# Optimization experiments

Hardware: AMD Instinct MI355X
Metric: run time of the kernel (lower is better)

## Reference

```python
import jax, jax.numpy as jnp
import numpy as np

P = 2.0  # exponent from init kwarg p


def _segment_mean(vals, idx, n):
    # scatter-mean with zero for empty segments (matches torch_scatter reduce='mean')
    s = jax.ops.segment_sum(vals, idx, num_segments=n)
    c = jax.ops.segment_sum(jnp.ones((vals.shape[0], 1), vals.dtype), idx, num_segments=n)
    return s / jnp.maximum(c, 1.0)


def setup_inputs() -> dict:
    key = jax.random.key(0)
    ks = jax.random.split(key, 6)
    N, E, nhid, heads = 100000, 3200000, 64, 4
    X = jax.random.normal(ks[0], (N, nhid), dtype=jnp.float32)
    edge_index = jax.random.randint(ks[1], (2, E), 0, N, dtype=jnp.int32)
    s1 = 1.0 / np.sqrt(nhid)
    W_self = jax.random.normal(ks[2], (nhid, nhid), dtype=jnp.float32) * s1
    W_neigh = jax.random.normal(ks[3], (nhid, nhid), dtype=jnp.float32) * s1
    b_conv = jnp.zeros((nhid,), dtype=jnp.float32)
    s2 = 1.0 / np.sqrt(2 * nhid)
    Qw = jax.random.normal(ks[4], (heads, 2 * nhid, nhid // heads), dtype=jnp.float32) * s2
    Qb = jnp.zeros((heads, nhid // heads), dtype=jnp.float32)
    return {"X": X, "edge_index": edge_index, "W_self": W_self,
            "W_neigh": W_neigh, "b_conv": b_conv, "Qw": Qw, "Qb": Qb}


def reference(X, edge_index, W_self, W_neigh, b_conv, Qw, Qb):
    N = X.shape[0]
    src, dst = edge_index[0], edge_index[1]
    # GraphSAGE conv: self-linear + linear over mean of neighbor features, then ReLU
    agg = _segment_mean(X[src], dst, N)                     # [N, nhid]
    X2 = jax.nn.relu(X @ W_self + agg @ W_neigh + b_conv)   # [N, nhid]
    # gather both edge endpoints and concat
    ef = jnp.concatenate([X2[src], X2[dst]], axis=1)        # [E, 2*nhid]
    # per-head small linear, abs^p, heads concatenated -> [E, nhid]
    h = jnp.einsum('ef,hfd->ehd', ef, Qw) + Qb              # [E, heads, nhid/heads]
    h = (jnp.abs(h) ** P).reshape(ef.shape[0], -1)
    # scatter-mean by source node, tanh
    gg = jnp.tanh(_segment_mean(h, src, N))                 # [N, nhid]
    return gg
```

## Files before the change

### kernel.cpp

```cpp
#include <hip/hip_runtime.h>
#include <math.h>

#define NHID 64
#define NPB 512
#define NPB_SHIFT 9
#define MAXB 256
#define CAP 20480
#define CHUNK 8192

__device__ __forceinline__ float bf_lo(unsigned u) { return __uint_as_float(u << 16); }
__device__ __forceinline__ float bf_hi(unsigned u) { return __uint_as_float(u & 0xffff0000u); }
__device__ __forceinline__ unsigned f2bf(float f) {
    unsigned u = __float_as_uint(f);
    return (u + 0x7fffu + ((u >> 16) & 1u)) >> 16;
}

__global__ __launch_bounds__(256) void k_bucketA(const int* __restrict__ src,
                                                 const int* __restrict__ dst,
                                                 unsigned int* __restrict__ buf0,
                                                 unsigned int* __restrict__ buf1,
                                                 int* __restrict__ btail0,
                                                 int* __restrict__ btail1,
                                                 int E, int nB, int nChunks) {
    int side  = blockIdx.x & 1;
    int chunk = blockIdx.x >> 1;
    const int* key = side ? src : dst;
    const int* pay = side ? dst : src;
    unsigned int* buf = side ? buf1 : buf0;
    int* btail = side ? btail1 : btail0;

    __shared__ int h[MAXB], b[MAXB];
    int tid = threadIdx.x;
    for (int i = tid; i < nB; i += 256) h[i] = 0;
    __syncthreads();
    int e0 = chunk * CHUNK;
    for (int i = tid; i < CHUNK / 4; i += 256) {
        int e = e0 + i * 4;
        if (e + 3 < E) {
            int4 k4 = ((const int4*)(key + e0))[i];
            atomicAdd(&h[k4.x >> NPB_SHIFT], 1);
            atomicAdd(&h[k4.y >> NPB_SHIFT], 1);
            atomicAdd(&h[k4.z >> NPB_SHIFT], 1);
            atomicAdd(&h[k4.w >> NPB_SHIFT], 1);
        } else {
            for (int j = 0; j < 4; ++j) {
                int e2 = e + j;
                if (e2 < E) atomicAdd(&h[key[e2] >> NPB_SHIFT], 1);
            }
        }
    }
    __syncthreads();
    for (int i = tid; i < nB; i += 256) {
        int c = h[i];
        b[i] = c ? atomicAdd(&btail[i], c) : 0;
        h[i] = 0;
    }
    __syncthreads();
    for (int i = tid; i < CHUNK / 4; i += 256) {
        int e = e0 + i * 4;
        if (e + 3 < E) {
            int4 k4 = ((const int4*)(key + e0))[i];
            int4 p4 = ((const int4*)(pay + e0))[i];
            int bb, r;
            bb = k4.x >> NPB_SHIFT; r = atomicAdd(&h[bb], 1) + b[bb];
            if (r < CAP) buf[(size_t)bb * CAP + r] = ((unsigned)p4.x << NPB_SHIFT) | (unsigned)(k4.x & (NPB - 1));
            bb = k4.y >> NPB_SHIFT; r = atomicAdd(&h[bb], 1) + b[bb];
            if (r < CAP) buf[(size_t)bb * CAP + r] = ((unsigned)p4.y << NPB_SHIFT) | (unsigned)(k4.y & (NPB - 1));
            bb = k4.z >> NPB_SHIFT; r = atomicAdd(&h[bb], 1) + b[bb];
            if (r < CAP) buf[(size_t)bb * CAP + r] = ((unsigned)p4.z << NPB_SHIFT) | (unsigned)(k4.z & (NPB - 1));
            bb = k4.w >> NPB_SHIFT; r = atomicAdd(&h[bb], 1) + b[bb];
            if (r < CAP) buf[(size_t)bb * CAP + r] = ((unsigned)p4.w << NPB_SHIFT) | (unsigned)(k4.w & (NPB - 1));
        } else {
            for (int j = 0; j < 4; ++j) {
                int e2 = e + j;
                if (e2 < E) {
                    int k = key[e2], p = pay[e2];
                    int bb = k >> NPB_SHIFT;
                    int r = atomicAdd(&h[bb], 1) + b[bb];
                    if (r < CAP) buf[(size_t)bb * CAP + r] = ((unsigned)p << NPB_SHIFT) | (unsigned)(k & (NPB - 1));
                }
            }
        }
    }
}

__global__ __launch_bounds__(256) void k_bscan(const int* __restrict__ btail0,
                                               const int* __restrict__ btail1,
                                               int* __restrict__ boff0, int* __restrict__ boff1,
                                               int* __restrict__ off0, int* __restrict__ off1,
                                               int nB, int N) {
    __shared__ int sd[256];
    int tid = threadIdx.x;
    int v = (tid < nB) ? min(btail0[tid], CAP) : 0;
    sd[tid] = v; __syncthreads();
    for (int o = 1; o < 256; o <<= 1) {
        int t = (tid >= o) ? sd[tid - o] : 0; __syncthreads();
        sd[tid] += t; __syncthreads();
    }
    if (tid < nB) boff0[tid] = sd[tid] - v;
    if (tid == 255) off0[N] = sd[255];
    __syncthreads();
    v = (tid < nB) ? min(btail1[tid], CAP) : 0;
    sd[tid] = v; __syncthreads();
    for (int o = 1; o < 256; o <<= 1) {
        int t = (tid >= o) ? sd[tid - o] : 0; __syncthreads();
        sd[tid] += t; __syncthreads();
    }
    if (tid < nB) boff1[tid] = sd[tid] - v;
    if (tid == 255) off1[N] = sd[255];
}

__global__ __launch_bounds__(512) void k_bucket_csr(const unsigned int* __restrict__ buf0,
                                                    const unsigned int* __restrict__ buf1,
                                                    const int* __restrict__ btail0,
                                                    const int* __restrict__ btail1,
                                                    const int* __restrict__ boff0,
                                                    const int* __restrict__ boff1,
                                                    int* __restrict__ off0, int* __restrict__ off1,
                                                    int* __restrict__ csr0, int* __restrict__ csr1,
                                                    int N) {
    int side = blockIdx.x & 1;
    int b = blockIdx.x >> 1;
    const unsigned int* buf = (side ? buf1 : buf0) + (size_t)b * CAP;
    int cnt_b = min((side ? btail1 : btail0)[b], CAP);
    int boff  = (side ? boff1 : boff0)[b];
    int* off  = side ? off1 : off0;
    int* csr  = side ? csr1 : csr0;
    __shared__ int cnt[NPB];
    __shared__ int scn[NPB];
    __shared__ int cur[NPB];
    int tid = threadIdx.x;
    cnt[tid] = 0;
    __syncthreads();
    for (int i = tid; i < cnt_b; i += 512)
        atomicAdd(&cnt[buf[i] & (NPB - 1)], 1);
    __syncthreads();
    int v = cnt[tid];
    scn[tid] = v; __syncthreads();
    for (int o = 1; o < 512; o <<= 1) {
        int t = (tid >= o) ? scn[tid - o] : 0; __syncthreads();
        scn[tid] += t; __syncthreads();
    }
    int base = boff + scn[tid] - v;
    cur[tid] = base;
    int node = (b << NPB_SHIFT) + tid;
    if (node < N) off[node] = base;
    __syncthreads();
    for (int i = tid; i < cnt_b; i += 512) {
        unsigned int u = buf[i];
        int pos = atomicAdd(&cur[u & (NPB - 1)], 1);
        csr[pos] = (int)(u >> NPB_SHIFT);
    }
}

__global__ __launch_bounds__(256) void k_xcast(const float* __restrict__ X,
                                               unsigned* __restrict__ Xb, int total8) {
    int i = blockIdx.x * 256 + threadIdx.x;
    if (i >= total8) return;
    const float4* Xv = (const float4*)X;
    float4 f0 = Xv[(size_t)i * 2];
    float4 f1 = Xv[(size_t)i * 2 + 1];
    uint4 p;
    p.x = f2bf(f0.x) | (f2bf(f0.y) << 16);
    p.y = f2bf(f0.z) | (f2bf(f0.w) << 16);
    p.z = f2bf(f1.x) | (f2bf(f1.y) << 16);
    p.w = f2bf(f1.z) | (f2bf(f1.w) << 16);
    ((uint4*)Xb)[i] = p;
}

__global__ __launch_bounds__(256) void k_agg(const unsigned* __restrict__ Xb,
                                             const int* __restrict__ off_dst,
                                             const int* __restrict__ csr_dst,
                                             float* __restrict__ agg, int N) {
    int lane = threadIdx.x & 63;
    int node = blockIdx.x * 4 + (threadIdx.x >> 6);
    if (node >= N) return;
    int grp = lane >> 3, col8 = lane & 7;
    const uint4* Xb4 = (const uint4*)Xb;
    int s0 = off_dst[node], s1 = off_dst[node + 1];
    float4 accA = make_float4(0.f, 0.f, 0.f, 0.f);
    float4 accB = make_float4(0.f, 0.f, 0.f, 0.f);
    for (int base = s0; base < s1; base += 64) {
        int cnt = min(64, s1 - base);
        int idx = (base + lane < s1) ? csr_dst[base + lane] : 0;
        int jfull = cnt & ~15;
        for (int j = 0; j < jfull; j += 16) {
            int m0 = __shfl(idx, j + grp);
            int m1 = __shfl(idx, j + 8 + grp);
            uint4 u0 = Xb4[(size_t)m0 * 8 + col8];
            uint4 u1 = Xb4[(size_t)m1 * 8 + col8];
            accA.x += bf_lo(u0.x); accA.y += bf_hi(u0.x);
            accA.z += bf_lo(u0.y); accA.w += bf_hi(u0.y);
            accB.x += bf_lo(u0.z); accB.y += bf_hi(u0.z);
            accB.z += bf_lo(u0.w); accB.w += bf_hi(u0.w);
            accA.x += bf_lo(u1.x); accA.y += bf_hi(u1.x);
            accA.z += bf_lo(u1.y); accA.w += bf_hi(u1.y);
            accB.x += bf_lo(u1.z); accB.y += bf_hi(u1.z);
            accB.z += bf_lo(u1.w); accB.w += bf_hi(u1.w);
        }
        if (jfull < cnt) {
            int q0 = jfull + grp, q1 = jfull + 8 + grp;
            int m0 = __shfl(idx, q0);
            int m1 = __shfl(idx, q1);
            float f0 = (q0 < cnt) ? 1.f : 0.f; if (q0 >= cnt) m0 = 0;
            float f1 = (q1 < cnt) ? 1.f : 0.f; if (q1 >= cnt) m1 = 0;
            uint4 u0 = Xb4[(size_t)m0 * 8 + col8];
            uint4 u1 = Xb4[(size_t)m1 * 8 + col8];
            accA.x += f0 * bf_lo(u0.x); accA.y += f0 * bf_hi(u0.x);
            accA.z += f0 * bf_lo(u0.y); accA.w += f0 * bf_hi(u0.y);
            accB.x += f0 * bf_lo(u0.z); accB.y += f0 * bf_hi(u0.z);
            accB.z += f0 * bf_lo(u0.w); accB.w += f0 * bf_hi(u0.w);
            accA.x += f1 * bf_lo(u1.x); accA.y += f1 * bf_hi(u1.x);
            accA.z += f1 * bf_lo(u1.y); accA.w += f1 * bf_hi(u1.y);
            accB.x += f1 * bf_lo(u1.z); accB.y += f1 * bf_hi(u1.z);
            accB.z += f1 * bf_lo(u1.w); accB.w += f1 * bf_hi(u1.w);
        }
    }
    #pragma unroll
    for (int d = 8; d < 64; d <<= 1) {
        accA.x += __shfl_xor(accA.x, d); accA.y += __shfl_xor(accA.y, d);
        accA.z += __shfl_xor(accA.z, d); accA.w += __shfl_xor(accA.w, d);
        accB.x += __shfl_xor(accB.x, d); accB.y += __shfl_xor(accB.y, d);
        accB.z += __shfl_xor(accB.z, d); accB.w += __shfl_xor(accB.w, d);
    }
    if (grp == 0) {
        int deg = s1 - s0;
        float inv = 1.f / (float)max(deg, 1);
        float4 r0 = make_float4(accA.x * inv, accA.y * inv, accA.z * inv, accA.w * inv);
        float4 r1 = make_float4(accB.x * inv, accB.y * inv, accB.z * inv, accB.w * inv);
        ((float4*)agg)[(size_t)node * 16 + col8 * 2]     = r0;
        ((float4*)agg)[(size_t)node * 16 + col8 * 2 + 1] = r1;
    }
}

__global__ __launch_bounds__(256) void k_phaseA(const float* __restrict__ X,
                                                const float* agg,
                                                const float* __restrict__ Ws,
                                                const float* __restrict__ Wn,
                                                const float* __restrict__ bconv,
                                                float* X2, int N) {
    __shared__ float sWs[4096];
    __shared__ float sWn[4096];
    __shared__ float sb[64];
    int tid = threadIdx.x;
    for (int i = tid; i < 4096; i += 256) {
        sWs[i] = Ws[i];
        sWn[i] = Wn[i];
    }
    if (tid < 64) sb[tid] = bconv[tid];
    __syncthreads();

    int n = blockIdx.x * 64 + (tid >> 2);
    if (n >= N) return;
    int wb = (tid & 3) << 2;
    const float4* ws4 = (const float4*)sWs;
    const float4* wn4 = (const float4*)sWn;
    const float4* bv  = (const float4*)sb;
    const float4* Xv  = (const float4*)(X + (size_t)n * NHID);
    const float4* Gv  = (const float4*)(agg + (size_t)n * NHID);
    float4 a0 = bv[wb], a1 = bv[wb + 1], a2 = bv[wb + 2], a3 = bv[wb + 3];
    #pragma unroll 2
    for (int q = 0; q < 16; ++q) {
        float4 xq = Xv[q];
        float4 gq = Gv[q];
        float xs[4] = {xq.x, xq.y, xq.z, xq.w};
        float gs[4] = {gq.x, gq.y, gq.z, gq.w};
        #pragma unroll
        for (int j = 0; j < 4; ++j) {
            int k16 = (4 * q + j) * 16 + wb;
            float4 w0 = ws4[k16], w1 = ws4[k16 + 1], w2 = ws4[k16 + 2], w3 = ws4[k16 + 3];
            float4 m0 = wn4[k16], m1 = wn4[k16 + 1], m2 = wn4[k16 + 2], m3 = wn4[k16 + 3];
            float xj = xs[j], gj = gs[j];
            a0.x += xj * w0.x + gj * m0.x; a0.y += xj * w0.y + gj * m0.y;
            a0.z += xj * w0.z + gj * m0.z; a0.w += xj * w0.w + gj * m0.w;
            a1.x += xj * w1.x + gj * m1.x; a1.y += xj * w1.y + gj * m1.y;
            a1.z += xj * w1.z + gj * m1.z; a1.w += xj * w1.w + gj * m1.w;
            a2.x += xj * w2.x + gj * m2.x; a2.y += xj * w2.y + gj * m2.y;
            a2.z += xj * w2.z + gj * m2.z; a2.w += xj * w2.w + gj * m2.w;
            a3.x += xj * w3.x + gj * m3.x; a3.y += xj * w3.y + gj * m3.y;
            a3.z += xj * w3.z + gj * m3.z; a3.w += xj * w3.w + gj * m3.w;
        }
    }
    float4* out = (float4*)(X2 + (size_t)n * NHID);
    out[wb]     = make_float4(fmaxf(a0.x, 0.f), fmaxf(a0.y, 0.f), fmaxf(a0.z, 0.f), fmaxf(a0.w, 0.f));
    out[wb + 1] = make_float4(fmaxf(a1.x, 0.f), fmaxf(a1.y, 0.f), fmaxf(a1.z, 0.f), fmaxf(a1.w, 0.f));
    out[wb + 2] = make_float4(fmaxf(a2.x, 0.f), fmaxf(a2.y, 0.f), fmaxf(a2.z, 0.f), fmaxf(a2.w, 0.f));
    out[wb + 3] = make_float4(fmaxf(a3.x, 0.f), fmaxf(a3.y, 0.f), fmaxf(a3.z, 0.f), fmaxf(a3.w, 0.f));
}

__global__ __launch_bounds__(256) void k_repackB(const float* __restrict__ Qw,
                                                 float* __restrict__ W2) {
    int i = blockIdx.x * 256 + threadIdx.x;
    if (i >= 8192) return;
    int f = i >> 7, c = i & 127;
    float v;
    if (c < 64) v = Qw[(c >> 4) * 2048 + f * 16 + (c & 15)];
    else { int cc = c - 64; v = Qw[(cc >> 4) * 2048 + (64 + f) * 16 + (cc & 15)]; }
    W2[i] = v;
}

__global__ __launch_bounds__(256) void k_phaseB(const float* __restrict__ X2,
                                                const float* __restrict__ W2,
                                                const float* __restrict__ Qb,
                                                float* __restrict__ aOut,
                                                unsigned* __restrict__ bOut, int N) {
    __shared__ float sW[8192];
    int tid = threadIdx.x;
    for (int i = tid; i < 8192; i += 256) sW[i] = W2[i];
    __syncthreads();

    int n = blockIdx.x * 32 + (tid >> 3);
    if (n >= N) return;
    int part = tid & 7;
    int wb = part << 2;
    const float4* w4 = (const float4*)sW;
    float4 a0, a1, a2, a3;
    if (part < 4) {
        const float4* qv = (const float4*)Qb;
        a0 = qv[wb]; a1 = qv[wb + 1]; a2 = qv[wb + 2]; a3 = qv[wb + 3];
    } else {
        a0 = a1 = a2 = a3 = make_float4(0.f, 0.f, 0.f, 0.f);
    }
    const float4* Xv = (const float4*)(X2 + (size_t)n * NHID);
    #pragma unroll 2
    for (int q = 0; q < 16; ++q) {
        float4 xq = Xv[q];
        float xs[4] = {xq.x, xq.y, xq.z, xq.w};
        #pragma unroll
        for (int j = 0; j < 4; ++j) {
            int f32b = (4 * q + j) * 32 + wb;
            float4 w0 = w4[f32b], w1 = w4[f32b + 1], w2 = w4[f32b + 2], w3 = w4[f32b + 3];
            float xj = xs[j];
            a0.x += xj * w0.x; a0.y += xj * w0.y; a0.z += xj * w0.z; a0.w += xj * w0.w;
            a1.x += xj * w1.x; a1.y += xj * w1.y; a1.z += xj * w1.z; a1.w += xj * w1.w;
            a2.x += xj * w2.x; a2.y += xj * w2.y; a2.z += xj * w2.z; a2.w += xj * w2.w;
            a3.x += xj * w3.x; a3.y += xj * w3.y; a3.z += xj * w3.z; a3.w += xj * w3.w;
        }
    }
    if (part < 4) {
        float4* outp = (float4*)(aOut + (size_t)n * NHID) + wb;
        outp[0] = a0; outp[1] = a1; outp[2] = a2; outp[3] = a3;
    } else {
        uint4 p0, p1;
        p0.x = f2bf(a0.x) | (f2bf(a0.y) << 16);
        p0.y = f2bf(a0.z) | (f2bf(a0.w) << 16);
        p0.z = f2bf(a1.x) | (f2bf(a1.y) << 16);
        p0.w = f2bf(a1.z) | (f2bf(a1.w) << 16);
        p1.x = f2bf(a2.x) | (f2bf(a2.y) << 16);
        p1.y = f2bf(a2.z) | (f2bf(a2.w) << 16);
        p1.z = f2bf(a3.x) | (f2bf(a3.y) << 16);
        p1.w = f2bf(a3.z) | (f2bf(a3.w) << 16);
        uint4* outp = (uint4*)bOut + (size_t)n * 8 + (part - 4) * 2;
        outp[0] = p0; outp[1] = p1;
    }
}

__global__ __launch_bounds__(256) void k_final(const float* __restrict__ aF,
                                               const unsigned* __restrict__ bFb,
                                               const int* __restrict__ off_src,
                                               const int* __restrict__ csr_src,
                                               float* __restrict__ out, int N) {
    int lane = threadIdx.x & 63;
    int node = blockIdx.x * 4 + (threadIdx.x >> 6);
    if (node >= N) return;
    int grp = lane >> 3, col8 = lane & 7;
    const uint4* Bv = (const uint4*)bFb;
    const float4* Av = (const float4*)aF;
    float4 avA = Av[(size_t)node * 16 + col8 * 2];
    float4 avB = Av[(size_t)node * 16 + col8 * 2 + 1];
    int s0 = off_src[node], s1 = off_src[node + 1];
    float4 accA = make_float4(0.f, 0.f, 0.f, 0.f);
    float4 accB = make_float4(0.f, 0.f, 0.f, 0.f);
    for (int base = s0; base < s1; base += 64) {
        int cnt = min(64, s1 - base);
        int idx = (base + lane < s1) ? csr_src[base + lane] : 0;
        int jfull = cnt & ~15;
        for (int j = 0; j < jfull; j += 16) {
            int m0 = __shfl(idx, j + grp);
            int m1 = __shfl(idx, j + 8 + grp);
            uint4 u0 = Bv[(size_t)m0 * 8 + col8];
            uint4 u1 = Bv[(size_t)m1 * 8 + col8];
            float t;
            t = avA.x + bf_lo(u0.x); accA.x += t * t;
            t = avA.y + bf_hi(u0.x); accA.y += t * t;
            t = avA.z + bf_lo(u0.y); accA.z += t * t;
            t = avA.w + bf_hi(u0.y); accA.w += t * t;
            t = avB.x + bf_lo(u0.z); accB.x += t * t;
            t = avB.y + bf_hi(u0.z); accB.y += t * t;
            t = avB.z + bf_lo(u0.w); accB.z += t * t;
            t = avB.w + bf_hi(u0.w); accB.w += t * t;
            t = avA.x + bf_lo(u1.x); accA.x += t * t;
            t = avA.y + bf_hi(u1.x); accA.y += t * t;
            t = avA.z + bf_lo(u1.y); accA.z += t * t;
            t = avA.w + bf_hi(u1.y); accA.w += t * t;
            t = avB.x + bf_lo(u1.z); accB.x += t * t;
            t = avB.y + bf_hi(u1.z); accB.y += t * t;
            t = avB.z + bf_lo(u1.w); accB.z += t * t;
            t = avB.w + bf_hi(u1.w); accB.w += t * t;
        }
        if (jfull < cnt) {
            int q0 = jfull + grp, q1 = jfull + 8 + grp;
            int m0 = __shfl(idx, q0);
            int m1 = __shfl(idx, q1);
            float f0 = (q0 < cnt) ? 1.f : 0.f; if (q0 >= cnt) m0 = 0;
            float f1 = (q1 < cnt) ? 1.f : 0.f; if (q1 >= cnt) m1 = 0;
            uint4 u0 = Bv[(size_t)m0 * 8 + col8];
            uint4 u1 = Bv[(size_t)m1 * 8 + col8];
            float t;
            t = avA.x + bf_lo(u0.x); accA.x += f0 * t * t;
            t = avA.y + bf_hi(u0.x); accA.y += f0 * t * t;
            t = avA.z + bf_lo(u0.y); accA.z += f0 * t * t;
            t = avA.w + bf_hi(u0.y); accA.w += f0 * t * t;
            t = avB.x + bf_lo(u0.z); accB.x += f0 * t * t;
            t = avB.y + bf_hi(u0.z); accB.y += f0 * t * t;
            t = avB.z + bf_lo(u0.w); accB.z += f0 * t * t;
            t = avB.w + bf_hi(u0.w); accB.w += f0 * t * t;
            t = avA.x + bf_lo(u1.x); accA.x += f1 * t * t;
            t = avA.y + bf_hi(u1.x); accA.y += f1 * t * t;
            t = avA.z + bf_lo(u1.y); accA.z += f1 * t * t;
            t = avA.w + bf_hi(u1.y); accA.w += f1 * t * t;
            t = avB.x + bf_lo(u1.z); accB.x += f1 * t * t;
            t = avB.y + bf_hi(u1.z); accB.y += f1 * t * t;
            t = avB.z + bf_lo(u1.w); accB.z += f1 * t * t;
            t = avB.w + bf_hi(u1.w); accB.w += f1 * t * t;
        }
    }
    #pragma unroll
    for (int d = 8; d < 64; d <<= 1) {
        accA.x += __shfl_xor(accA.x, d); accA.y += __shfl_xor(accA.y, d);
        accA.z += __shfl_xor(accA.z, d); accA.w += __shfl_xor(accA.w, d);
        accB.x += __shfl_xor(accB.x, d); accB.y += __shfl_xor(accB.y, d);
        accB.z += __shfl_xor(accB.z, d); accB.w += __shfl_xor(accB.w, d);
    }
    if (grp == 0) {
        int deg = s1 - s0;
        float inv = 1.f / (float)max(deg, 1);
        float4 r0 = make_float4(tanhf(accA.x * inv), tanhf(accA.y * inv),
                                tanhf(accA.z * inv), tanhf(accA.w * inv));
        float4 r1 = make_float4(tanhf(accB.x * inv), tanhf(accB.y * inv),
                                tanhf(accB.z * inv), tanhf(accB.w * inv));
        ((float4*)out)[(size_t)node * 16 + col8 * 2]     = r0;
        ((float4*)out)[(size_t)node * 16 + col8 * 2 + 1] = r1;
    }
}

extern "C" void kernel_launch(void* const* d_in, const int* in_sizes, int n_in,
                              void* d_out, int out_size, void* d_ws, size_t ws_size,
                              hipStream_t stream) {
    const float* X      = (const float*)d_in[0];
    const int*   ei     = (const int*)d_in[1];
    const float* Wself  = (const float*)d_in[2];
    const float* Wneigh = (const float*)d_in[3];
    const float* bconv  = (const float*)d_in[4];
    const float* Qw     = (const float*)d_in[5];
    const float* Qb     = (const float*)d_in[6];

    int N = in_sizes[0] / NHID;
    int E = in_sizes[1] / 2;
    const int* src = ei;
    const int* dst = ei + E;
    int nB = (N + NPB - 1) >> NPB_SHIFT;
    int nChunks = (E + CHUNK - 1) / CHUNK;

    char* ws = (char*)d_ws;
    size_t bufBytes = (size_t)MAXB * CAP * 4;
    size_t NH4 = (size_t)N * NHID * 4;
    size_t NH2 = (size_t)N * NHID * 2;
    unsigned int* buf0 = (unsigned int*)(ws);
    unsigned int* buf1 = (unsigned int*)(ws + bufBytes);
    float*    aggF = (float*)(ws);
    float*    aF   = (float*)(ws + NH4);
    unsigned* bFb  = (unsigned*)(ws + 2 * NH4);
    unsigned* Xb   = (unsigned*)(ws + 2 * NH4 + NH2);
    size_t pos = 3 * NH4;
    if (pos < 2 * bufBytes) pos = 2 * bufBytes;
    pos = (pos + 255) & ~(size_t)255;
    auto alloc = [&](size_t bytes) -> void* {
        void* p = ws + pos;
        pos = (pos + bytes + 255) & ~(size_t)255;
        return p;
    };
    int* csr0   = (int*)alloc((size_t)E * 4);
    int* csr1   = (int*)alloc((size_t)E * 4);
    int* off0   = (int*)alloc((size_t)(N + 1) * 4);
    int* off1   = (int*)alloc((size_t)(N + 1) * 4);
    int* btail0 = (int*)alloc((size_t)MAXB * 4);
    int* btail1 = (int*)alloc((size_t)MAXB * 4);
    int* boff0  = (int*)alloc((size_t)MAXB * 4);
    int* boff1  = (int*)alloc((size_t)MAXB * 4);
    float* W2   = (float*)alloc((size_t)8192 * 4);
    (void)ws_size; (void)n_in; (void)out_size;

    hipMemsetAsync(btail0, 0, (size_t)2 * MAXB * 4, stream);

    k_bucketA<<<nChunks * 2, 256, 0, stream>>>(src, dst, buf0, buf1, btail0, btail1,
                                               E, nB, nChunks);
    k_bscan<<<1, 256, 0, stream>>>(btail0, btail1, boff0, boff1, off0, off1, nB, N);
    k_repackB<<<32, 256, 0, stream>>>(Qw, W2);
    k_xcast<<<(N * 8 + 255) / 256, 256, 0, stream>>>(X, Xb, N * 8);
    k_bucket_csr<<<nB * 2, 512, 0, stream>>>(buf0, buf1, btail0, btail1,
                                             boff0, boff1, off0, off1, csr0, csr1, N);
    k_agg<<<(N + 3) / 4, 256, 0, stream>>>(Xb, off0, csr0, aggF, N);
    k_phaseA<<<(N + 63) / 64, 256, 0, stream>>>(X, aggF, Wself, Wneigh, bconv, aggF, N);
    k_phaseB<<<(N + 31) / 32, 256, 0, stream>>>(aggF, W2, Qb, aF, bFb, N);
    k_final<<<(N + 3) / 4, 256, 0, stream>>>(aF, bFb, off1, csr1, (float*)d_out, N);
}
```

Baseline: 329.6 us.

## Store X2 and per-node head projections in bf16 and unroll gathers by four

The ReLU output X2 and the per-node 'a' projection are now stored as packed bf16 instead of fp32, which halves intermediate traffic between phaseA, phaseB and the final edge kernel. The neighbor gather loops in k_agg and k_final now process 32 edges per iteration instead of 16, which puts more loads in flight per wave. The unused nChunks argument is dropped, and X2 is written to its own buffer instead of overwriting the aggregate in place. The cost is extra bf16 rounding on X2 and on the 'a' term before squaring, which adds numerical error.

```diff
diff --git a/kernel.cpp b/kernel.cpp
--- a/kernel.cpp
+++ b/kernel.cpp
@@ -21,7 +21,7 @@
                                                  unsigned int* __restrict__ buf1,
                                                  int* __restrict__ btail0,
                                                  int* __restrict__ btail1,
-                                                 int E, int nB, int nChunks) {
+                                                 int E, int nB) {
     int side  = blockIdx.x & 1;
     int chunk = blockIdx.x >> 1;
     const int* key = side ? src : dst;
@@ -168,6 +168,17 @@
     ((uint4*)Xb)[i] = p;
 }
 
+#define AGG_ACC(u) \
+    accA.x += bf_lo(u.x); accA.y += bf_hi(u.x); \
+    accA.z += bf_lo(u.y); accA.w += bf_hi(u.y); \
+    accB.x += bf_lo(u.z); accB.y += bf_hi(u.z); \
+    accB.z += bf_lo(u.w); accB.w += bf_hi(u.w);
+#define AGG_ACCM(u, f) \
+    accA.x += f * bf_lo(u.x); accA.y += f * bf_hi(u.x); \
+    accA.z += f * bf_lo(u.y); accA.w += f * bf_hi(u.y); \
+    accB.x += f * bf_lo(u.z); accB.y += f * bf_hi(u.z); \
+    accB.z += f * bf_lo(u.w); accB.w += f * bf_hi(u.w);
+
 __global__ __launch_bounds__(256) void k_agg(const unsigned* __restrict__ Xb,
                                              const int* __restrict__ off_dst,
                                              const int* __restrict__ csr_dst,
@@ -183,37 +194,33 @@
     for (int base = s0; base < s1; base += 64) {
         int cnt = min(64, s1 - base);
         int idx = (base + lane < s1) ? csr_dst[base + lane] : 0;
-        int jfull = cnt & ~15;
-        for (int j = 0; j < jfull; j += 16) {
+        int j = 0;
+        for (; j + 32 <= cnt; j += 32) {
             int m0 = __shfl(idx, j + grp);
             int m1 = __shfl(idx, j + 8 + grp);
+            int m2 = __shfl(idx, j + 16 + grp);
+            int m3 = __shfl(idx, j + 24 + grp);
             uint4 u0 = Xb4[(size_t)m0 * 8 + col8];
             uint4 u1 = Xb4[(size_t)m1 * 8 + col8];
-            accA.x += bf_lo(u0.x); accA.y += bf_hi(u0.x);
-            accA.z += bf_lo(u0.y); accA.w += bf_hi(u0.y);
-            accB.x += bf_lo(u0.z); accB.y += bf_hi(u0.z);
-            accB.z += bf_lo(u0.w); accB.w += bf_hi(u0.w);
-            accA.x += bf_lo(u1.x); accA.y += bf_hi(u1.x);
-            accA.z += bf_lo(u1.y); accA.w += bf_hi(u1.y);
-            accB.x += bf_lo(u1.z); accB.y += bf_hi(u1.z);
-            accB.z += bf_lo(u1.w); accB.w += bf_hi(u1.w);
-        }
-        if (jfull < cnt) {
-            int q0 = jfull + grp, q1 = jfull + 8 + grp;
+            uint4 u2 = Xb4[(size_t)m2 * 8 + col8];
+            uint4 u3 = Xb4[(size_t)m3 * 8 + col8];
+            AGG_ACC(u0); AGG_ACC(u1); AGG_ACC(u2); AGG_ACC(u3);
+        }
+        if (j < cnt) {
+            int q0 = j + grp, q1 = j + 8 + grp, q2 = j + 16 + grp, q3 = j + 24 + grp;
             int m0 = __shfl(idx, q0);
             int m1 = __shfl(idx, q1);
+            int m2 = __shfl(idx, q2);
+            int m3 = __shfl(idx, q3);
             float f0 = (q0 < cnt) ? 1.f : 0.f; if (q0 >= cnt) m0 = 0;
             float f1 = (q1 < cnt) ? 1.f : 0.f; if (q1 >= cnt) m1 = 0;
+            float f2 = (q2 < cnt) ? 1.f : 0.f; if (q2 >= cnt) m2 = 0;
+            float f3 = (q3 < cnt) ? 1.f : 0.f; if (q3 >= cnt) m3 = 0;
             uint4 u0 = Xb4[(size_t)m0 * 8 + col8];
             uint4 u1 = Xb4[(size_t)m1 * 8 + col8];
-            accA.x += f0 * bf_lo(u0.x); accA.y += f0 * bf_hi(u0.x);
-            accA.z += f0 * bf_lo(u0.y); accA.w += f0 * bf_hi(u0.y);
-            accB.x += f0 * bf_lo(u0.z); accB.y += f0 * bf_hi(u0.z);
-            accB.z += f0 * bf_lo(u0.w); accB.w += f0 * bf_hi(u0.w);
-            accA.x += f1 * bf_lo(u1.x); accA.y += f1 * bf_hi(u1.x);
-            accA.z += f1 * bf_lo(u1.y); accA.w += f1 * bf_hi(u1.y);
-            accB.x += f1 * bf_lo(u1.z); accB.y += f1 * bf_hi(u1.z);
-            accB.z += f1 * bf_lo(u1.w); accB.w += f1 * bf_hi(u1.w);
+            uint4 u2 = Xb4[(size_t)m2 * 8 + col8];
+            uint4 u3 = Xb4[(size_t)m3 * 8 + col8];
+            AGG_ACCM(u0, f0); AGG_ACCM(u1, f1); AGG_ACCM(u2, f2); AGG_ACCM(u3, f3);
         }
     }
     #pragma unroll
@@ -234,11 +241,11 @@
 }
 
 __global__ __launch_bounds__(256) void k_phaseA(const float* __restrict__ X,
-                                                const float* agg,
+                                                const float* __restrict__ agg,
                                                 const float* __restrict__ Ws,
                                                 const float* __restrict__ Wn,
                                                 const float* __restrict__ bconv,
-                                                float* X2, int N) {
+                                                unsigned* __restrict__ X2b, int N) {
     __shared__ float sWs[4096];
     __shared__ float sWn[4096];
     __shared__ float sb[64];
@@ -281,11 +288,21 @@
             a3.z += xj * w3.z + gj * m3.z; a3.w += xj * w3.w + gj * m3.w;
         }
     }
-    float4* out = (float4*)(X2 + (size_t)n * NHID);
-    out[wb]     = make_float4(fmaxf(a0.x, 0.f), fmaxf(a0.y, 0.f), fmaxf(a0.z, 0.f), fmaxf(a0.w, 0.f));
-    out[wb + 1] = make_float4(fmaxf(a1.x, 0.f), fmaxf(a1.y, 0.f), fmaxf(a1.z, 0.f), fmaxf(a1.w, 0.f));
-    out[wb + 2] = make_float4(fmaxf(a2.x, 0.f), fmaxf(a2.y, 0.f), fmaxf(a2.z, 0.f), fmaxf(a2.w, 0.f));
-    out[wb + 3] = make_float4(fmaxf(a3.x, 0.f), fmaxf(a3.y, 0.f), fmaxf(a3.z, 0.f), fmaxf(a3.w, 0.f));
+    a0.x = fmaxf(a0.x, 0.f); a0.y = fmaxf(a0.y, 0.f); a0.z = fmaxf(a0.z, 0.f); a0.w = fmaxf(a0.w, 0.f);
+    a1.x = fmaxf(a1.x, 0.f); a1.y = fmaxf(a1.y, 0.f); a1.z = fmaxf(a1.z, 0.f); a1.w = fmaxf(a1.w, 0.f);
+    a2.x = fmaxf(a2.x, 0.f); a2.y = fmaxf(a2.y, 0.f); a2.z = fmaxf(a2.z, 0.f); a2.w = fmaxf(a2.w, 0.f);
+    a3.x = fmaxf(a3.x, 0.f); a3.y = fmaxf(a3.y, 0.f); a3.z = fmaxf(a3.z, 0.f); a3.w = fmaxf(a3.w, 0.f);
+    uint4 p0, p1;
+    p0.x = f2bf(a0.x) | (f2bf(a0.y) << 16);
+    p0.y = f2bf(a0.z) | (f2bf(a0.w) << 16);
+    p0.z = f2bf(a1.x) | (f2bf(a1.y) << 16);
+    p0.w = f2bf(a1.z) | (f2bf(a1.w) << 16);
+    p1.x = f2bf(a2.x) | (f2bf(a2.y) << 16);
+    p1.y = f2bf(a2.z) | (f2bf(a2.w) << 16);
+    p1.z = f2bf(a3.x) | (f2bf(a3.y) << 16);
+    p1.w = f2bf(a3.z) | (f2bf(a3.w) << 16);
+    uint4* outp = (uint4*)X2b + (size_t)n * 8 + (tid & 3) * 2;
+    outp[0] = p0; outp[1] = p1;
 }
 
 __global__ __launch_bounds__(256) void k_repackB(const float* __restrict__ Qw,
@@ -299,10 +316,10 @@
     W2[i] = v;
 }
 
-__global__ __launch_bounds__(256) void k_phaseB(const float* __restrict__ X2,
+__global__ __launch_bounds__(256) void k_phaseB(const unsigned* __restrict__ X2b,
                                                 const float* __restrict__ W2,
                                                 const float* __restrict__ Qb,
-                                                float* __restrict__ aOut,
+                                                unsigned* __restrict__ aOut,
                                                 unsigned* __restrict__ bOut, int N) {
     __shared__ float sW[8192];
     int tid = threadIdx.x;
@@ -321,14 +338,15 @@
     } else {
         a0 = a1 = a2 = a3 = make_float4(0.f, 0.f, 0.f, 0.f);
     }
-    const float4* Xv = (const float4*)(X2 + (size_t)n * NHID);
+    const uint4* Xv = (const uint4*)((const uint4*)X2b + (size_t)n * 8);
     #pragma unroll 2
-    for (int q = 0; q < 16; ++q) {
-        float4 xq = Xv[q];
-        float xs[4] = {xq.x, xq.y, xq.z, xq.w};
+    for (int q8 = 0; q8 < 8; ++q8) {
+        uint4 xu = Xv[q8];
+        float xs[8] = {bf_lo(xu.x), bf_hi(xu.x), bf_lo(xu.y), bf_hi(xu.y),
+                       bf_lo(xu.z), bf_hi(xu.z), bf_lo(xu.w), bf_hi(xu.w)};
         #pragma unroll
-        for (int j = 0; j < 4; ++j) {
-            int f32b = (4 * q + j) * 32 + wb;
+        for (int j = 0; j < 8; ++j) {
+            int f32b = (8 * q8 + j) * 32 + wb;
             float4 w0 = w4[f32b], w1 = w4[f32b + 1], w2 = w4[f32b + 2], w3 = w4[f32b + 3];
             float xj = xs[j];
             a0.x += xj * w0.x; a0.y += xj * w0.y; a0.z += xj * w0.z; a0.w += xj * w0.w;
@@ -337,25 +355,40 @@
             a3.x += xj * w3.x; a3.y += xj * w3.y; a3.z += xj * w3.z; a3.w += xj * w3.w;
         }
     }
-    if (part < 4) {
-        float4* outp = (float4*)(aOut + (size_t)n * NHID) + wb;
-        outp[0] = a0; outp[1] = a1; outp[2] = a2; outp[3] = a3;
-    } else {
-        uint4 p0, p1;
-        p0.x = f2bf(a0.x) | (f2bf(a0.y) << 16);
-        p0.y = f2bf(a0.z) | (f2bf(a0.w) << 16);
-        p0.z = f2bf(a1.x) | (f2bf(a1.y) << 16);
-        p0.w = f2bf(a1.z) | (f2bf(a1.w) << 16);
-        p1.x = f2bf(a2.x) | (f2bf(a2.y) << 16);
-        p1.y = f2bf(a2.z) | (f2bf(a2.w) << 16);
-        p1.z = f2bf(a3.x) | (f2bf(a3.y) << 16);
-        p1.w = f2bf(a3.z) | (f2bf(a3.w) << 16);
-        uint4* outp = (uint4*)bOut + (size_t)n * 8 + (part - 4) * 2;
-        outp[0] = p0; outp[1] = p1;
-    }
-}
-
-__global__ __launch_bounds__(256) void k_final(const float* __restrict__ aF,
+    uint4 p0, p1;
+    p0.x = f2bf(a0.x) | (f2bf(a0.y) << 16);
+    p0.y = f2bf(a0.z) | (f2bf(a0.w) << 16);
+    p0.z = f2bf(a1.x) | (f2bf(a1.y) << 16);
+    p0.w = f2bf(a1.z) | (f2bf(a1.w) << 16);
+    p1.x = f2bf(a2.x) | (f2bf(a2.y) << 16);
+    p1.y = f2bf(a2.z) | (f2bf(a2.w) << 16);
+    p1.z = f2bf(a3.x) | (f2bf(a3.y) << 16);
+    p1.w = f2bf(a3.z) | (f2bf(a3.w) << 16);
+    uint4* outp = (part < 4) ? (uint4*)aOut + (size_t)n * 8 + part * 2
+                             : (uint4*)bOut + (size_t)n * 8 + (part - 4) * 2;
+    outp[0] = p0; outp[1] = p1;
+}
+
+#define FIN_ACC(u) { float t; \
+    t = avA.x + bf_lo(u.x); accA.x += t * t; \
+    t = avA.y + bf_hi(u.x); accA.y += t * t; \
+    t = avA.z + bf_lo(u.y); accA.z += t * t; \
+    t = avA.w + bf_hi(u.y); accA.w += t * t; \
+    t = avB.x + bf_lo(u.z); accB.x += t * t; \
+    t = avB.y + bf_hi(u.z); accB.y += t * t; \
+    t = avB.z + bf_lo(u.w); accB.z += t * t; \
+    t = avB.w + bf_hi(u.w); accB.w += t * t; }
+#define FIN_ACCM(u, f) { float t; \
+    t = avA.x + bf_lo(u.x); accA.x += f * t * t; \
+    t = avA.y + bf_hi(u.x); accA.y += f * t * t; \
+    t = avA.z + bf_lo(u.y); accA.z += f * t * t; \
+    t = avA.w + bf_hi(u.y); accA.w += f * t * t; \
+    t = avB.x + bf_lo(u.z); accB.x += f * t * t; \
+    t = avB.y + bf_hi(u.z); accB.y += f * t * t; \
+    t = avB.z + bf_lo(u.w); accB.z += f * t * t; \
+    t = avB.w + bf_hi(u.w); accB.w += f * t * t; }
+
+__global__ __launch_bounds__(256) void k_final(const unsigned* __restrict__ aFb,
                                                const unsigned* __restrict__ bFb,
                                                const int* __restrict__ off_src,
                                                const int* __restrict__ csr_src,
@@ -365,64 +398,42 @@
     if (node >= N) return;
     int grp = lane >> 3, col8 = lane & 7;
     const uint4* Bv = (const uint4*)bFb;
-    const float4* Av = (const float4*)aF;
-    float4 avA = Av[(size_t)node * 16 + col8 * 2];
-    float4 avB = Av[(size_t)node * 16 + col8 * 2 + 1];
+    uint4 au = ((const uint4*)aFb)[(size_t)node * 8 + col8];
+    float4 avA = make_float4(bf_lo(au.x), bf_hi(au.x), bf_lo(au.y), bf_hi(au.y));
+    float4 avB = make_float4(bf_lo(au.z), bf_hi(au.z), bf_lo(au.w), bf_hi(au.w));
     int s0 = off_src[node], s1 = off_src[node + 1];
     float4 accA = make_float4(0.f, 0.f, 0.f, 0.f);
     float4 accB = make_float4(0.f, 0.f, 0.f, 0.f);
     for (int base = s0; base < s1; base += 64) {
         int cnt = min(64, s1 - base);
         int idx = (base + lane < s1) ? csr_src[base + lane] : 0;
-        int jfull = cnt & ~15;
-        for (int j = 0; j < jfull; j += 16) {
+        int j = 0;
+        for (; j + 32 <= cnt; j += 32) {
             int m0 = __shfl(idx, j + grp);
             int m1 = __shfl(idx, j + 8 + grp);
+            int m2 = __shfl(idx, j + 16 + grp);
+            int m3 = __shfl(idx, j + 24 + grp);
             uint4 u0 = Bv[(size_t)m0 * 8 + col8];
             uint4 u1 = Bv[(size_t)m1 * 8 + col8];
-            float t;
-            t = avA.x + bf_lo(u0.x); accA.x += t * t;
-            t = avA.y + bf_hi(u0.x); accA.y += t * t;
-            t = avA.z + bf_lo(u0.y); accA.z += t * t;
-            t = avA.w + bf_hi(u0.y); accA.w += t * t;
-            t = avB.x + bf_lo(u0.z); accB.x += t * t;
-            t = avB.y + bf_hi(u0.z); accB.y += t * t;
-            t = avB.z + bf_lo(u0.w); accB.z += t * t;
-            t = avB.w + bf_hi(u0.w); accB.w += t * t;
-            t = avA.x + bf_lo(u1.x); accA.x += t * t;
-            t = avA.y + bf_hi(u1.x); accA.y += t * t;
-            t = avA.z + bf_lo(u1.y); accA.z += t * t;
-            t = avA.w + bf_hi(u1.y); accA.w += t * t;
-            t = avB.x + bf_lo(u1.z); accB.x += t * t;
-            t = avB.y + bf_hi(u1.z); accB.y += t * t;
-            t = avB.z + bf_lo(u1.w); accB.z += t * t;
-            t = avB.w + bf_hi(u1.w); accB.w += t * t;
-        }
-        if (jfull < cnt) {
-            int q0 = jfull + grp, q1 = jfull + 8 + grp;
+            uint4 u2 = Bv[(size_t)m2 * 8 + col8];
+            uint4 u3 = Bv[(size_t)m3 * 8 + col8];
+            FIN_ACC(u0); FIN_ACC(u1); FIN_ACC(u2); FIN_ACC(u3);
+        }
+        if (j < cnt) {
+            int q0 = j + grp, q1 = j + 8 + grp, q2 = j + 16 + grp, q3 = j + 24 + grp;
             int m0 = __shfl(idx, q0);
             int m1 = __shfl(idx, q1);
+            int m2 = __shfl(idx, q2);
+            int m3 = __shfl(idx, q3);
             float f0 = (q0 < cnt) ? 1.f : 0.f; if (q0 >= cnt) m0 = 0;
             float f1 = (q1 < cnt) ? 1.f : 0.f; if (q1 >= cnt) m1 = 0;
+            float f2 = (q2 < cnt) ? 1.f : 0.f; if (q2 >= cnt) m2 = 0;
+            float f3 = (q3 < cnt) ? 1.f : 0.f; if (q3 >= cnt) m3 = 0;
             uint4 u0 = Bv[(size_t)m0 * 8 + col8];
             uint4 u1 = Bv[(size_t)m1 * 8 + col8];
-            float t;
-            t = avA.x + bf_lo(u0.x); accA.x += f0 * t * t;
-            t = avA.y + bf_hi(u0.x); accA.y += f0 * t * t;
-            t = avA.z + bf_lo(u0.y); accA.z += f0 * t * t;
-            t = avA.w + bf_hi(u0.y); accA.w += f0 * t * t;
-            t = avB.x + bf_lo(u0.z); accB.x += f0 * t * t;
-            t = avB.y + bf_hi(u0.z); accB.y += f0 * t * t;
-            t = avB.z + bf_lo(u0.w); accB.z += f0 * t * t;
-            t = avB.w + bf_hi(u0.w); accB.w += f0 * t * t;
-            t = avA.x + bf_lo(u1.x); accA.x += f1 * t * t;
-            t = avA.y + bf_hi(u1.x); accA.y += f1 * t * t;
-            t = avA.z + bf_lo(u1.y); accA.z += f1 * t * t;
-            t = avA.w + bf_hi(u1.y); accA.w += f1 * t * t;
-            t = avB.x + bf_lo(u1.z); accB.x += f1 * t * t;
-            t = avB.y + bf_hi(u1.z); accB.y += f1 * t * t;
-            t = avB.z + bf_lo(u1.w); accB.z += f1 * t * t;
-            t = avB.w + bf_hi(u1.w); accB.w += f1 * t * t;
+            uint4 u2 = Bv[(size_t)m2 * 8 + col8];
+            uint4 u3 = Bv[(size_t)m3 * 8 + col8];
+            FIN_ACCM(u0, f0); FIN_ACCM(u1, f1); FIN_ACCM(u2, f2); FIN_ACCM(u3, f3);
         }
     }
     #pragma unroll
@@ -469,10 +480,11 @@
     unsigned int* buf0 = (unsigned int*)(ws);
     unsigned int* buf1 = (unsigned int*)(ws + bufBytes);
     float*    aggF = (float*)(ws);
-    float*    aF   = (float*)(ws + NH4);
-    unsigned* bFb  = (unsigned*)(ws + 2 * NH4);
-    unsigned* Xb   = (unsigned*)(ws + 2 * NH4 + NH2);
-    size_t pos = 3 * NH4;
+    unsigned* X2b  = (unsigned*)(ws + NH4);
+    unsigned* aFb  = (unsigned*)(ws + NH4 + NH2);
+    unsigned* bFb  = (unsigned*)(ws + NH4 + 2 * NH2);
+    unsigned* Xb   = (unsigned*)(ws + NH4 + 3 * NH2);
+    size_t pos = NH4 + 4 * NH2;
     if (pos < 2 * bufBytes) pos = 2 * bufBytes;
     pos = (pos + 255) & ~(size_t)255;
     auto alloc = [&](size_t bytes) -> void* {
@@ -493,15 +505,14 @@
 
     hipMemsetAsync(btail0, 0, (size_t)2 * MAXB * 4, stream);
 
-    k_bucketA<<<nChunks * 2, 256, 0, stream>>>(src, dst, buf0, buf1, btail0, btail1,
-                                               E, nB, nChunks);
+    k_bucketA<<<nChunks * 2, 256, 0, stream>>>(src, dst, buf0, buf1, btail0, btail1, E, nB);
     k_bscan<<<1, 256, 0, stream>>>(btail0, btail1, boff0, boff1, off0, off1, nB, N);
     k_repackB<<<32, 256, 0, stream>>>(Qw, W2);
     k_xcast<<<(N * 8 + 255) / 256, 256, 0, stream>>>(X, Xb, N * 8);
     k_bucket_csr<<<nB * 2, 512, 0, stream>>>(buf0, buf1, btail0, btail1,
                                              boff0, boff1, off0, off1, csr0, csr1, N);
     k_agg<<<(N + 3) / 4, 256, 0, stream>>>(Xb, off0, csr0, aggF, N);
-    k_phaseA<<<(N + 63) / 64, 256, 0, stream>>>(X, aggF, Wself, Wneigh, bconv, aggF, N);
-    k_phaseB<<<(N + 31) / 32, 256, 0, stream>>>(aggF, W2, Qb, aF, bFb, N);
-    k_final<<<(N + 3) / 4, 256, 0, stream>>>(aF, bFb, off1, csr1, (float*)d_out, N);
-}
+    k_phaseA<<<(N + 63) / 64, 256, 0, stream>>>(X, aggF, Wself, Wneigh, bconv, X2b, N);
+    k_phaseB<<<(N + 31) / 32, 256, 0, stream>>>(X2b, W2, Qb, aFb, bFb, N);
+    k_final<<<(N + 3) / 4, 256, 0, stream>>>(aFb, bFb, off1, csr1, (float*)d_out, N);
+}
```

After: 329.6 us. About the same (+0.0%).
